# Optimization experiments

Measured on AMD Instinct MI355X. Metric: run time of the kernel, lower is better.

## Reference

```python
import jax, jax.numpy as jnp
import numpy as np

H = 1024  # hidden_dim
M = 4     # num_modalities
B = 8192  # batch


def setup_inputs() -> dict:
    key = jax.random.key(0)
    ks = jax.random.split(key, 10)
    s = 1.0 / np.sqrt(H)  # torch Linear default init scale
    return {
        "features": jax.random.normal(ks[0], (B, M, H), dtype=jnp.float32),
        "confidences": jax.random.uniform(ks[1], (B, M, 1), dtype=jnp.float32),
        "Wq": jax.random.uniform(ks[2], (H, H), jnp.float32, -s, s),
        "bq": jax.random.uniform(ks[3], (H,), jnp.float32, -s, s),
        "Wk": jax.random.uniform(ks[4], (H, H), jnp.float32, -s, s),
        "bk": jax.random.uniform(ks[5], (H,), jnp.float32, -s, s),
        "Wv": jax.random.uniform(ks[6], (H, H), jnp.float32, -s, s),
        "bv": jax.random.uniform(ks[7], (H,), jnp.float32, -s, s),
        "Wo": jax.random.uniform(ks[8], (H, H), jnp.float32, -s, s),
        "bo": jax.random.uniform(ks[9], (H,), jnp.float32, -s, s),
    }


def reference(features, confidences, Wq, bq, Wk, bk, Wv, bv, Wo, bo):
    # features: [B, M, H], confidences: [B, M, 1]
    q = jnp.einsum('bmh,oh->bmo', features, Wq) + bq
    k = jnp.einsum('bmh,oh->bmo', features, Wk) + bk
    v = jnp.einsum('bmh,oh->bmo', features, Wv) + bv
    scores = jnp.einsum('bmh,bnh->bmn', q, k) / jnp.sqrt(jnp.float32(features.shape[-1]))
    scores = scores * confidences  # [B,M,1] broadcasts over last (key) axis
    attn = jax.nn.softmax(scores, axis=-1)           # [B, M, M]
    attended = jnp.einsum('bmn,bnh->bmh', attn, v)   # [B, M, H]
    fused = jnp.mean(attended, axis=1)               # [B, H]
    return fused @ Wo.T + bo
```

## Files before the change

kernel.cpp:

```cpp
#include <hip/hip_runtime.h>


typedef unsigned short u16;
typedef unsigned char u8;
typedef __attribute__((ext_vector_type(8))) __bf16 bf16x8;
typedef __attribute__((ext_vector_type(4))) float floatx4;

__device__ __forceinline__ u16 f2bf(float f) {
    unsigned u = __float_as_uint(f);
    unsigned r = (u + 0x7FFFu + ((u >> 16) & 1u)) >> 16;
    return (u16)r;
}

__device__ __forceinline__ unsigned f2e4m3(float x) {
    unsigned u = __float_as_uint(x);
    unsigned s = (u >> 31) << 7;
    float a = __uint_as_float(u & 0x7FFFFFFFu);
    if (a >= 448.f) return s | 0x7E;
    if (a < 0.03125f) {
        unsigned k = (unsigned)__float2int_rn(a * 512.f);
        return s | k;
    }
    unsigned b = __float_as_uint(a);
    unsigned lsb = (b >> 20) & 1u;
    b += 0x0007FFFFu + lsb;
    unsigned ex = (b >> 23) - 120u;
    unsigned man = (b >> 20) & 7u;
    return s | (ex << 3) | man;
}

__device__ __forceinline__ void load_lds16(const void* g, void* l) {
    __builtin_amdgcn_global_load_lds(
        (const __attribute__((address_space(1))) void*)g,
        (__attribute__((address_space(3))) void*)l, 16, 0, 0);
}

__device__ __forceinline__ void unpack8(uint4 v, float* f) {
    f[0] = __uint_as_float(v.x << 16);
    f[1] = __uint_as_float(v.x & 0xFFFF0000u);
    f[2] = __uint_as_float(v.y << 16);
    f[3] = __uint_as_float(v.y & 0xFFFF0000u);
    f[4] = __uint_as_float(v.z << 16);
    f[5] = __uint_as_float(v.z & 0xFFFF0000u);
    f[6] = __uint_as_float(v.w << 16);
    f[7] = __uint_as_float(v.w & 0xFFFF0000u);
}

__global__ __launch_bounds__(256) void k_cast(const float* __restrict__ in,
                                              u16* __restrict__ outb,
                                              u8* __restrict__ outf, long n) {
    long i = ((long)blockIdx.x * 256 + threadIdx.x) * 4;
    if (i < n) {
        float4 v = *(const float4*)(in + i);
        ushort4 o;
        o.x = f2bf(v.x); o.y = f2bf(v.y); o.z = f2bf(v.z); o.w = f2bf(v.w);
        *(ushort4*)(outb + i) = o;
        if (outf) {
            unsigned p = f2e4m3(v.x) | (f2e4m3(v.y) << 8) |
                         (f2e4m3(v.z) << 16) | (f2e4m3(v.w) << 24);
            *(unsigned*)(outf + i) = p;
        }
    }
}

__global__ __launch_bounds__(256) void k_prep(const float* __restrict__ Wq,
                                              const float* __restrict__ Wk,
                                              const float* __restrict__ Wv,
                                              const float* __restrict__ Wo,
                                              u16* __restrict__ WqT,
                                              u16* __restrict__ WkT,
                                              u16* __restrict__ WvT,
                                              u16* __restrict__ Wob, int H) {
    __shared__ float t[32][33];
    const int z = blockIdx.z;
    const float* in = (z == 0) ? Wk : (z == 1) ? Wq : (z == 2) ? Wv : Wo;
    u16* out = (z == 0) ? WkT : (z == 1) ? WqT : (z == 2) ? WvT : Wob;
    int bx = blockIdx.x * 32, by = blockIdx.y * 32;
    int x = threadIdx.x;
    if (z < 3) {
        for (int y = threadIdx.y; y < 32; y += 8)
            t[y][x] = in[(size_t)(by + y) * H + bx + x];
        __syncthreads();
        for (int y = threadIdx.y; y < 32; y += 8)
            out[(size_t)(bx + y) * H + by + x] = f2bf(t[x][y]);
    } else {
        for (int y = threadIdx.y; y < 32; y += 8)
            out[(size_t)(by + y) * H + bx + x] = f2bf(in[(size_t)(by + y) * H + bx + x]);
    }
}

__global__ __launch_bounds__(256) void k_uk(const float* __restrict__ Wk,
                                            const float* __restrict__ bq,
                                            float* __restrict__ u, int H) {
    int h = blockIdx.x * 256 + threadIdx.x;
    int chunk = H / 16;
    int o0 = blockIdx.y * chunk;
    float s = 0.f;
    for (int o = o0; o < o0 + chunk; ++o) s += bq[o] * Wk[(size_t)o * H + h];
    atomicAdd(&u[h], s);
}

__global__ __launch_bounds__(256) void k_bias(const float* __restrict__ Wo,
                                              const float* __restrict__ bv,
                                              const float* __restrict__ bo,
                                              float* __restrict__ c, int H) {
    __shared__ float red[4];
    int j = blockIdx.x;
    int lane = threadIdx.x & 63, wv = threadIdx.x >> 6;
    float s = 0.f;
    for (int o = threadIdx.x; o < H; o += 256) s += Wo[(size_t)j * H + o] * bv[o];
    for (int off = 32; off > 0; off >>= 1) s += __shfl_down(s, off);
    if (lane == 0) red[wv] = s;
    __syncthreads();
    if (threadIdx.x == 0) c[j] = red[0] + red[1] + red[2] + red[3] + bo[j];
}

template <int OUTMODE>
__device__ __forceinline__ void gemm_body(const u16* __restrict__ A,
                                          const u16* __restrict__ Bw,
                                          void* __restrict__ Cp,
                                          u8* __restrict__ Cp8,
                                          const float* __restrict__ bias,
                                          int M, int N, int K,
                                          int bx, int by) {
    __shared__ __align__(16) u16 As[128 * 32];
    __shared__ __align__(16) u16 Bs[128 * 32];
    const int tid = threadIdx.x, lane = tid & 63, wv = tid >> 6;
    const int m0 = bx * 128, n0 = by * 128;
    const int wm = (wv >> 1) * 64, wn = (wv & 1) * 64;

    floatx4 acc[4][4];
#pragma unroll
    for (int i = 0; i < 4; ++i)
#pragma unroll
        for (int j = 0; j < 4; ++j) acc[i][j] = (floatx4){0.f, 0.f, 0.f, 0.f};

    const int srow = lane >> 2;
    const int scol = (((lane & 3) ^ ((lane >> 3) & 3)) * 8);
    const u16* gA = A + (size_t)(m0 + srow) * K + scol;
    const u16* gB = Bw + (size_t)(n0 + srow) * K + scol;
    const int r = lane & 15, q = lane >> 4;
    const int cph = q ^ ((r >> 1) & 3);

    for (int kt = 0; kt < K; kt += 32) {
#pragma unroll
        for (int c = 0; c < 2; ++c) {
            int chunk = wv * 2 + c;
            load_lds16(gA + (size_t)(chunk * 16) * K + kt, &As[chunk * 16 * 32]);
            load_lds16(gB + (size_t)(chunk * 16) * K + kt, &Bs[chunk * 16 * 32]);
        }
        __syncthreads();
        bf16x8 af[4], bfr[4];
#pragma unroll
        for (int i = 0; i < 4; ++i) {
            af[i] = *(const bf16x8*)&As[(wm + i * 16 + r) * 32 + cph * 8];
            bfr[i] = *(const bf16x8*)&Bs[(wn + i * 16 + r) * 32 + cph * 8];
        }
#pragma unroll
        for (int i = 0; i < 4; ++i)
#pragma unroll
            for (int j = 0; j < 4; ++j)
                acc[i][j] = __builtin_amdgcn_mfma_f32_16x16x32_bf16(af[i], bfr[j], acc[i][j], 0, 0, 0);
        __syncthreads();
    }

    const int cc = lane & 15, cr = (lane >> 4) * 4;
#pragma unroll
    for (int i = 0; i < 4; ++i)
#pragma unroll
        for (int j = 0; j < 4; ++j) {
            int col = n0 + wn + j * 16 + cc;
            float badd = bias ? bias[col] : 0.f;
#pragma unroll
            for (int r0 = 0; r0 < 4; ++r0) {
                int row = m0 + wm + i * 16 + cr + r0;
                float v = acc[i][j][r0] + badd;
                if (OUTMODE == 0) ((float*)Cp)[(size_t)row * N + col] = v;
                else ((u16*)Cp)[(size_t)row * N + col] = f2bf(v);
                if (OUTMODE == 2)
                    Cp8[(size_t)row * N + col] = (u8)f2e4m3(32.f * v);
            }
        }
}

__global__ __launch_bounds__(256) void k_wgemm(const u16* __restrict__ A0,
                                               const u16* __restrict__ B0,
                                               u16* __restrict__ C0,
                                               u8* __restrict__ C0f8,
                                               const u16* __restrict__ A1,
                                               const u16* __restrict__ B1,
                                               u16* __restrict__ C1, int H) {
    if (blockIdx.z == 0)
        gemm_body<2>(A0, B0, C0, C0f8, nullptr, H, H, H, blockIdx.x, blockIdx.y);
    else
        gemm_body<1>(A1, B1, C1, nullptr, nullptr, H, H, H, blockIdx.x, blockIdx.y);
}

__global__ __launch_bounds__(256) void k_score(const u16* __restrict__ X,
                                               const u16* __restrict__ Aw,
                                               u16* __restrict__ G,
                                               const float* __restrict__ uk,
                                               int Mr, int N, int K) {
    gemm_body<1>(X, Aw, G, nullptr, uk, Mr, N, K, blockIdx.x, blockIdx.y);
}

__global__ __launch_bounds__(256) void k_out(const u16* __restrict__ A,
                                             const u16* __restrict__ Bw,
                                             float* __restrict__ C,
                                             const float* __restrict__ bias,
                                             int M, int N, int K) {
    gemm_body<0>(A, Bw, C, nullptr, bias, M, N, K, blockIdx.x, blockIdx.y);
}

__global__ __launch_bounds__(256) void k_score8(const u8* __restrict__ Af8,
                                                const u8* __restrict__ Bf8,
                                                u16* __restrict__ G,
                                                const float* __restrict__ uk,
                                                int Mr, int N, int K) {
    __shared__ __align__(16) u8 As[128 * 64];
    __shared__ __align__(16) u8 Bs[128 * 64];
    const int tid = threadIdx.x, lane = tid & 63, wv = tid >> 6;
    const int n0 = blockIdx.x * 128, m0 = blockIdx.y * 128;
    const int wm = (wv >> 1) * 64, wn = (wv & 1) * 64;

    floatx4 acc[4][4];
#pragma unroll
    for (int i = 0; i < 4; ++i)
#pragma unroll
        for (int j = 0; j < 4; ++j) acc[i][j] = (floatx4){0.f, 0.f, 0.f, 0.f};

    const int srow = lane >> 2;
    const int scol = 16 * ((lane & 3) ^ ((lane >> 3) & 3));
    const u8* gA = Af8 + (size_t)(m0 + srow) * K + scol;
    const u8* gB = Bf8 + (size_t)(n0 + srow) * K + scol;
    const int r = lane & 15, q = lane >> 4;
    const int swz = (r >> 1) & 3;
    const int qh = q >> 1, ql = (q & 1) * 8;

    for (int kt = 0; kt < K; kt += 64) {
#pragma unroll
        for (int c = 0; c < 2; ++c) {
            int chunk = wv * 2 + c;
            load_lds16(gA + (size_t)(chunk * 16) * K + kt, &As[chunk * 16 * 64]);
            load_lds16(gB + (size_t)(chunk * 16) * K + kt, &Bs[chunk * 16 * 64]);
        }
        __syncthreads();
#pragma unroll
        for (int s = 0; s < 2; ++s) {
            long long af[4], bfr[4];
#pragma unroll
            for (int i = 0; i < 4; ++i) {
                int piece = ((2 * s + qh) ^ swz) * 16 + ql;
                af[i] = *(const long long*)&As[(wm + i * 16 + r) * 64 + piece];
                bfr[i] = *(const long long*)&Bs[(wn + i * 16 + r) * 64 + piece];
            }
#pragma unroll
            for (int i = 0; i < 4; ++i)
#pragma unroll
                for (int j = 0; j < 4; ++j)
                    acc[i][j] = __builtin_amdgcn_mfma_f32_16x16x32_fp8_fp8(
                        af[i], bfr[j], acc[i][j], 0, 0, 0);
        }
        __syncthreads();
    }

    const int cc = lane & 15, cr = (lane >> 4) * 4;
#pragma unroll
    for (int i = 0; i < 4; ++i)
#pragma unroll
        for (int j = 0; j < 4; ++j) {
            int col = n0 + wn + j * 16 + cc;
            float badd = 32.f * uk[col];
#pragma unroll
            for (int r0 = 0; r0 < 4; ++r0) {
                int row = m0 + wm + i * 16 + cr + r0;
                G[(size_t)row * N + col] = f2bf(acc[i][j][r0] + badd);
            }
        }
}

__global__ __launch_bounds__(256) void k_attn(const u16* __restrict__ G,
                                              const u16* __restrict__ X,
                                              const float* __restrict__ conf,
                                              u16* __restrict__ Y, float gscale,
                                              int H) {
    const int lane = threadIdx.x & 63, wv = threadIdx.x >> 6;
    const int b = blockIdx.x * 4 + wv;
    const u16* Gb = G + (size_t)b * 4 * H;
    const u16* Xb = X + (size_t)b * 4 * H;

    uint4 xraw[2][4];
    float s[16];
#pragma unroll
    for (int t = 0; t < 16; ++t) s[t] = 0.f;

#pragma unroll
    for (int c = 0; c < 2; ++c) {
        const int off = c * 512 + lane * 8;
#pragma unroll
        for (int rr = 0; rr < 4; ++rr)
            xraw[c][rr] = *(const uint4*)(Xb + rr * H + off);
        float xv[4][8];
#pragma unroll
        for (int rr = 0; rr < 4; ++rr) unpack8(xraw[c][rr], xv[rr]);
#pragma unroll
        for (int m = 0; m < 4; ++m) {
            uint4 gl = *(const uint4*)(Gb + m * H + off);
            float gv[8];
            unpack8(gl, gv);
#pragma unroll
            for (int n = 0; n < 4; ++n) {
                float a = 0.f;
#pragma unroll
                for (int j = 0; j < 8; ++j) a += gv[j] * xv[n][j];
                s[m * 4 + n] += a;
            }
        }
    }
#pragma unroll
    for (int t = 0; t < 16; ++t) {
#pragma unroll
        for (int mask = 32; mask; mask >>= 1) s[t] += __shfl_xor(s[t], mask);
    }
    float w[4] = {0.f, 0.f, 0.f, 0.f};
#pragma unroll
    for (int m = 0; m < 4; ++m) {
        float cm = conf[(size_t)b * 4 + m] * gscale;
        float sc[4], mx = -1e30f;
#pragma unroll
        for (int n = 0; n < 4; ++n) {
            sc[n] = s[m * 4 + n] * cm;
            mx = fmaxf(mx, sc[n]);
        }
        float e[4], ssum = 0.f;
#pragma unroll
        for (int n = 0; n < 4; ++n) { e[n] = __expf(sc[n] - mx); ssum += e[n]; }
        float inv = 0.25f / ssum;
#pragma unroll
        for (int n = 0; n < 4; ++n) w[n] += e[n] * inv;
    }
#pragma unroll
    for (int c = 0; c < 2; ++c) {
        const int off = c * 512 + lane * 8;
        float xv[4][8];
#pragma unroll
        for (int rr = 0; rr < 4; ++rr) unpack8(xraw[c][rr], xv[rr]);
        float y[8];
#pragma unroll
        for (int j = 0; j < 8; ++j)
            y[j] = w[0] * xv[0][j] + w[1] * xv[1][j] + w[2] * xv[2][j] + w[3] * xv[3][j];
        uint4 res;
        res.x = (unsigned)f2bf(y[0]) | ((unsigned)f2bf(y[1]) << 16);
        res.y = (unsigned)f2bf(y[2]) | ((unsigned)f2bf(y[3]) << 16);
        res.z = (unsigned)f2bf(y[4]) | ((unsigned)f2bf(y[5]) << 16);
        res.w = (unsigned)f2bf(y[6]) | ((unsigned)f2bf(y[7]) << 16);
        *(uint4*)(Y + (size_t)b * H + off) = res;
    }
}

extern "C" void kernel_launch(void* const* d_in, const int* in_sizes, int n_in,
                              void* d_out, int out_size, void* d_ws, size_t ws_size,
                              hipStream_t stream) {
    const int H = 1024, M = 4;
    const int B = in_sizes[0] / (H * M);
    const long BMH = (long)B * M * H;

    const float* feat = (const float*)d_in[0];
    const float* conf = (const float*)d_in[1];
    const float* Wq = (const float*)d_in[2];
    const float* bq = (const float*)d_in[3];
    const float* Wk = (const float*)d_in[4];
    const float* Wv = (const float*)d_in[6];
    const float* bv = (const float*)d_in[7];
    const float* Wo = (const float*)d_in[8];
    const float* bo = (const float*)d_in[9];

    char* ws = (char*)d_ws;
    size_t off = 0;
    auto alloc = [&](size_t bytes) {
        void* p = ws + off;
        off += (bytes + 255) & ~(size_t)255;
        return p;
    };
    u16* Xb    = (u16*)alloc((size_t)BMH * 2);
    u16* G     = (u16*)alloc((size_t)BMH * 2);
    u16* Yb    = (u16*)alloc((size_t)B * H * 2);
    u16* WkT   = (u16*)alloc((size_t)H * H * 2);
    u16* WqT   = (u16*)alloc((size_t)H * H * 2);
    u16* WvT   = (u16*)alloc((size_t)H * H * 2);
    u16* Wob   = (u16*)alloc((size_t)H * H * 2);
    u16* Aw    = (u16*)alloc((size_t)H * H * 2);
    u16* Wov   = (u16*)alloc((size_t)H * H * 2);
    float* u    = (float*)alloc((size_t)H * 4);
    float* cvec = (float*)alloc((size_t)H * 4);
    u8* Xf8  = (u8*)alloc((size_t)BMH);
    u8* Awf8 = (u8*)alloc((size_t)H * H);
    const bool use_fp8 = (off <= ws_size);
    (void)n_in; (void)out_size;

    k_cast<<<(int)(BMH / 4 / 256), 256, 0, stream>>>(
        feat, Xb, use_fp8 ? Xf8 : nullptr, BMH);
    k_prep<<<dim3(H / 32, H / 32, 4), dim3(32, 8), 0, stream>>>(
        Wq, Wk, Wv, Wo, WqT, WkT, WvT, Wob, H);

    hipMemsetAsync(u, 0, (size_t)H * 4, stream);
    k_uk<<<dim3(H / 256, 16), 256, 0, stream>>>(Wk, bq, u, H);
    k_bias<<<H, 256, 0, stream>>>(Wo, bv, bo, cvec, H);

    k_wgemm<<<dim3(H / 128, H / 128, 2), 256, 0, stream>>>(
        WkT, WqT, Aw, use_fp8 ? Awf8 : (u8*)Aw , Wob, WvT, Wov, H);

    if (use_fp8) {
        k_score8<<<dim3(H / 128, B * M / 128), 256, 0, stream>>>(
            Xf8, Awf8, G, u, B * M, H, H);
    } else {
        k_score<<<dim3(B * M / 128, H / 128), 256, 0, stream>>>(
            Xb, Aw, G, u, B * M, H, H);
    }

    k_attn<<<B / 4, 256, 0, stream>>>(G, Xb, conf, Yb,
                                      use_fp8 ? 0.0009765625f : 0.03125f, H);

    k_out<<<dim3(B / 128, H / 128), 256, 0, stream>>>(Yb, Wov, (float*)d_out, cvec, B, H, H);
}
```

Measured before the change: 414.0 us.

## Use 32x32x64 scaled FP8 MFMA and XCD-aware block remap in score GEMM

The FP8 score GEMM swaps the 16x16x32 fp8 MFMA for the gfx950 scaled 32x32x64 f8f6f4 MFMA with unit scales. This cuts the instruction count and lets each lane read 16-byte LDS fragments instead of 8-byte ones. It also remaps workgroup IDs so that consecutive tiles land on the same XCD, which should improve L2 reuse. The risks are a mismatch in the output row mapping or LDS bank conflicts under the existing swizzle.

```diff
diff --git a/kernel.cpp b/kernel.cpp
--- a/kernel.cpp
+++ b/kernel.cpp
@@ -5,6 +5,8 @@
 typedef unsigned char u8;
 typedef __attribute__((ext_vector_type(8))) __bf16 bf16x8;
 typedef __attribute__((ext_vector_type(4))) float floatx4;
+typedef __attribute__((ext_vector_type(16))) float floatx16;
+typedef __attribute__((ext_vector_type(8))) int intx8;
 
 __device__ __forceinline__ u16 f2bf(float f) {
     unsigned u = __float_as_uint(f);
@@ -220,22 +222,33 @@
     __shared__ __align__(16) u8 As[128 * 64];
     __shared__ __align__(16) u8 Bs[128 * 64];
     const int tid = threadIdx.x, lane = tid & 63, wv = tid >> 6;
-    const int n0 = blockIdx.x * 128, m0 = blockIdx.y * 128;
+
+    const int nbx = gridDim.x;
+    const int nwg = nbx * gridDim.y;
+    const int orig = blockIdx.y * nbx + blockIdx.x;
+    const int cpx = nwg >> 3;
+    const int id = (orig & 7) * cpx + (orig >> 3);
+    const int n0 = (id % nbx) * 128, m0 = (id / nbx) * 128;
     const int wm = (wv >> 1) * 64, wn = (wv & 1) * 64;
 
-    floatx4 acc[4][4];
-#pragma unroll
-    for (int i = 0; i < 4; ++i)
-#pragma unroll
-        for (int j = 0; j < 4; ++j) acc[i][j] = (floatx4){0.f, 0.f, 0.f, 0.f};
+    floatx16 acc[2][2];
+#pragma unroll
+    for (int i = 0; i < 2; ++i)
+#pragma unroll
+        for (int j = 0; j < 2; ++j)
+            acc[i][j] = (floatx16){0.f, 0.f, 0.f, 0.f, 0.f, 0.f, 0.f, 0.f,
+                                   0.f, 0.f, 0.f, 0.f, 0.f, 0.f, 0.f, 0.f};
 
     const int srow = lane >> 2;
     const int scol = 16 * ((lane & 3) ^ ((lane >> 3) & 3));
     const u8* gA = Af8 + (size_t)(m0 + srow) * K + scol;
     const u8* gB = Bf8 + (size_t)(n0 + srow) * K + scol;
-    const int r = lane & 15, q = lane >> 4;
-    const int swz = (r >> 1) & 3;
-    const int qh = q >> 1, ql = (q & 1) * 8;
+
+    const int r32 = lane & 31, q2 = lane >> 5;
+    const int sw = (r32 >> 1) & 3;
+    const int c0 = (2 * q2) ^ sw, c1 = (2 * q2 + 1) ^ sw;
+
+    union frag32 { intx8 v; uint4 q[2]; };
 
     for (int kt = 0; kt < K; kt += 64) {
 #pragma unroll
@@ -245,36 +258,37 @@
             load_lds16(gB + (size_t)(chunk * 16) * K + kt, &Bs[chunk * 16 * 64]);
         }
         __syncthreads();
-#pragma unroll
-        for (int s = 0; s < 2; ++s) {
-            long long af[4], bfr[4];
-#pragma unroll
-            for (int i = 0; i < 4; ++i) {
-                int piece = ((2 * s + qh) ^ swz) * 16 + ql;
-                af[i] = *(const long long*)&As[(wm + i * 16 + r) * 64 + piece];
-                bfr[i] = *(const long long*)&Bs[(wn + i * 16 + r) * 64 + piece];
-            }
-#pragma unroll
-            for (int i = 0; i < 4; ++i)
-#pragma unroll
-                for (int j = 0; j < 4; ++j)
-                    acc[i][j] = __builtin_amdgcn_mfma_f32_16x16x32_fp8_fp8(
-                        af[i], bfr[j], acc[i][j], 0, 0, 0);
-        }
+        frag32 fa[2], fb[2];
+#pragma unroll
+        for (int i = 0; i < 2; ++i) {
+            const u8* pa = &As[(wm + i * 32 + r32) * 64];
+            const u8* pb = &Bs[(wn + i * 32 + r32) * 64];
+            fa[i].q[0] = *(const uint4*)(pa + c0 * 16);
+            fa[i].q[1] = *(const uint4*)(pa + c1 * 16);
+            fb[i].q[0] = *(const uint4*)(pb + c0 * 16);
+            fb[i].q[1] = *(const uint4*)(pb + c1 * 16);
+        }
+#pragma unroll
+        for (int i = 0; i < 2; ++i)
+#pragma unroll
+            for (int j = 0; j < 2; ++j)
+                acc[i][j] = __builtin_amdgcn_mfma_scale_f32_32x32x64_f8f6f4(
+                    fa[i].v, fb[j].v, acc[i][j], 0, 0,
+                    0, 0x7F7F7F7F, 0, 0x7F7F7F7F);
         __syncthreads();
     }
 
-    const int cc = lane & 15, cr = (lane >> 4) * 4;
-#pragma unroll
-    for (int i = 0; i < 4; ++i)
-#pragma unroll
-        for (int j = 0; j < 4; ++j) {
-            int col = n0 + wn + j * 16 + cc;
+    const int cc = lane & 31, rbase = 4 * (lane >> 5);
+#pragma unroll
+    for (int i = 0; i < 2; ++i)
+#pragma unroll
+        for (int j = 0; j < 2; ++j) {
+            int col = n0 + wn + j * 32 + cc;
             float badd = 32.f * uk[col];
 #pragma unroll
-            for (int r0 = 0; r0 < 4; ++r0) {
-                int row = m0 + wm + i * 16 + cr + r0;
-                G[(size_t)row * N + col] = f2bf(acc[i][j][r0] + badd);
+            for (int reg = 0; reg < 16; ++reg) {
+                int row = m0 + wm + i * 32 + (reg & 3) + 8 * (reg >> 2) + rbase;
+                G[(size_t)row * N + col] = f2bf(acc[i][j][reg] + badd);
             }
         }
 }
```

Measured after the change: 391.2 us. 5.5% less time.
